# Optimization experiments

Measured on AMD Instinct MI355X. Metric: run time of the kernel, lower is better.

## Reference

```python
import jax, jax.numpy as jnp
import numpy as np

B, N, F_IN = 8, 4096, 32
K = 40          # n_neighbours (includes self, which is dropped)
S = 4           # n_dimensions
P = 22          # n_propagate
F_OUT = 48      # n_filters


def setup_inputs() -> dict:
    key = jax.random.key(0)
    ks = jax.random.split(key, 7)
    def glorot(k, shape):
        fan_in = shape[0]
        return jax.random.normal(k, shape, jnp.float32) / np.sqrt(fan_in)
    x = jax.random.normal(ks[0], (B, N, F_IN), jnp.float32)
    Wf = glorot(ks[1], (F_IN, P)); bf = jnp.zeros((P,), jnp.float32)
    Ws = glorot(ks[2], (F_IN, S)); bs = jnp.zeros((S,), jnp.float32)
    Wo = glorot(ks[3], (F_IN + 2 * P, F_OUT)); bo = jnp.zeros((F_OUT,), jnp.float32)
    return {"x": x, "Wf": Wf, "bf": bf, "Ws": Ws, "bs": bs, "Wo": Wo, "bo": bo}


def reference(x, Wf, bf, Ws, bs, Wo, bo):
    # input transforms
    feats = x @ Wf + bf            # [B, N, P]
    coords = x @ Ws + bs           # [B, N, S]

    # pairwise squared euclidean distances  [B, N, N]
    sq = jnp.sum(coords * coords, axis=-1)
    d2 = sq[:, :, None] + sq[:, None, :] - 2.0 * jnp.einsum('bns,bms->bnm', coords, coords)

    # top-k nearest (top_k of -d2); entry 0 is the vertex itself -> drop it
    neg_d, idx = jax.lax.top_k(-d2, K)          # [B, N, K]
    nidx = idx[:, :, 1:]                         # [B, N, K-1]
    # distance as in TF code: ranked_distances (= -d2 values) sliced
    dist = neg_d[:, :, 1:]                       # negative squared distances

    # gather neighbour features: [B, N, K-1, P]
    neigh = jax.vmap(lambda f, i: f[i])(feats, nidx)

    # gauss_of_lin(dist * 10) = exp(-|dist * 10|)
    w = jnp.exp(-jnp.abs(dist * 10.0))[..., None]
    nf = neigh * w

    agg = jnp.concatenate([jnp.max(nf, axis=2), jnp.mean(nf, axis=2)], axis=-1)  # [B, N, 2P]
    updated = jnp.concatenate([x, agg], axis=-1)                                  # [B, N, F_IN+2P]
    return jnp.tanh(updated @ Wo + bo)                                            # [B, N, F_OUT]
```

## Files before the change

kernel.cpp:

```cpp
#include <hip/hip_runtime.h>
#include <cmath>

#define NN    4096
#define FIN   32
#define KSEL  39
#define PP    22
#define PPAD  24
#define FOUT  48
#define WPB   2
#define QW    4
#define CAP   128
#define WCOLS 32

#define WSYNC() asm volatile("s_waitcnt lgkmcnt(0)" ::: "memory")

__device__ __forceinline__ int lane_prefix(unsigned long long m) {
    return __builtin_amdgcn_mbcnt_hi((unsigned)(m >> 32),
           __builtin_amdgcn_mbcnt_lo((unsigned)m, 0));
}
__device__ __forceinline__ unsigned ford(float f) {
    int u = __float_as_int(f);
    return (u >= 0) ? ((unsigned)u | 0x80000000u) : ~(unsigned)u;
}
__device__ __forceinline__ float funord(unsigned k) {
    unsigned v = (k & 0x80000000u) ? (k & 0x7FFFFFFFu) : ~k;
    return __uint_as_float(v);
}
__device__ __forceinline__ float lane_bcast(float v, int l) {
    return __uint_as_float((unsigned)__builtin_amdgcn_readlane((int)__float_as_uint(v), l));
}
__device__ __forceinline__ float sq4(float4 c) {
    return fmaf(c.x, c.x, fmaf(c.y, c.y, fmaf(c.z, c.z, c.w * c.w)));
}

__global__ __launch_bounds__(256) void gn_pre(
    const float* __restrict__ x,
    const float* __restrict__ Wf, const float* __restrict__ bf,
    const float* __restrict__ Ws, const float* __restrict__ bs,
    float* __restrict__ coords4, float* __restrict__ feats)
{
    __shared__ __align__(16) float sW[FIN * WCOLS];
    __shared__ float sB[WCOLS];

    int t = threadIdx.x;
    for (int idx = t; idx < FIN * WCOLS; idx += 256) {
        int i = idx >> 5, c = idx & 31;
        float v = 0.f;
        if (c < PP) v = Wf[i * PP + c];
        else if (c >= 24 && c < 28) v = Ws[i * 4 + (c - 24)];
        sW[idx] = v;
    }
    if (t < WCOLS) {
        float v = 0.f;
        if (t < PP) v = bf[t];
        else if (t >= 24 && t < 28) v = bs[t - 24];
        sB[t] = v;
    }
    __syncthreads();

    int gid = blockIdx.x * 256 + t;
    int p = gid >> 2;
    int h = gid & 3;
    int c0 = h * 8;

    const float4* xr4 = (const float4*)(x + (size_t)p * FIN);
    float acc[8];
    #pragma unroll
    for (int k = 0; k < 8; ++k) acc[k] = sB[c0 + k];

    #pragma unroll
    for (int i = 0; i < 8; ++i) {
        float4 xt = xr4[i];
        const float* w0 = sW + (4 * i + 0) * WCOLS + c0;
        const float* w1 = sW + (4 * i + 1) * WCOLS + c0;
        const float* w2 = sW + (4 * i + 2) * WCOLS + c0;
        const float* w3 = sW + (4 * i + 3) * WCOLS + c0;
        #pragma unroll
        for (int k = 0; k < 8; ++k) acc[k] = fmaf(xt.x, w0[k], acc[k]);
        #pragma unroll
        for (int k = 0; k < 8; ++k) acc[k] = fmaf(xt.y, w1[k], acc[k]);
        #pragma unroll
        for (int k = 0; k < 8; ++k) acc[k] = fmaf(xt.z, w2[k], acc[k]);
        #pragma unroll
        for (int k = 0; k < 8; ++k) acc[k] = fmaf(xt.w, w3[k], acc[k]);
    }

    if (h < 3) {
        float4* fw = (float4*)(feats + (size_t)p * PPAD + c0);
        fw[0] = make_float4(acc[0], acc[1], acc[2], acc[3]);
        fw[1] = make_float4(acc[4], acc[5], acc[6], acc[7]);
    } else {
        ((float4*)coords4)[p] = make_float4(acc[0], acc[1], acc[2], acc[3]);
    }
}

__device__ __forceinline__ void sort64_pair(float& v, int& m, int lane) {
    #pragma unroll
    for (int k = 2; k <= 64; k <<= 1) {
        #pragma unroll
        for (int j = k >> 1; j >= 1; j >>= 1) {
            float ov = __shfl_xor(v, j);
            int   om = __shfl_xor(m, j);
            bool keepMin = (((lane & j) == 0) == ((lane & k) == 0));
            bool less = (ov < v) || (ov == v && om < m);
            bool take = (less == keepMin);
            v = take ? ov : v;
            m = take ? om : m;
        }
    }
}
__device__ __forceinline__ void merge64(float& Lv, int& Lm, float cv, int cm, int lane) {
    float rv = __shfl_xor(cv, 63);
    int   rm = __shfl_xor(cm, 63);
    bool less = (rv < Lv) || (rv == Lv && rm < Lm);
    if (less) { Lv = rv; Lm = rm; }
    #pragma unroll
    for (int j = 32; j >= 1; j >>= 1) {
        float ov = __shfl_xor(Lv, j);
        int   om = __shfl_xor(Lm, j);
        bool lower = ((lane & j) == 0);
        bool l2 = (ov < Lv) || (ov == Lv && om < Lm);
        bool take = (l2 == lower);
        Lv = take ? ov : Lv;
        Lm = take ? om : Lm;
    }
}

__device__ __forceinline__ float tail_select(
    int lane, int b, int nj, int C,
    const unsigned short* __restrict__ selq,
    const float4* __restrict__ c4,
    const float* __restrict__ feats,
    float* __restrict__ fstage)
{
    const float INF = __builtin_inff();
    float4 cqj = c4[nj];
    float sqnj = sq4(cqj);

    if (C <= CAP) {
        unsigned kd0 = 0xFFFFFFFFu, ki0 = 0xFFFFFFFFu; float dv0 = 0.f;
        if (lane < C) {
            unsigned idx = (unsigned)selq[lane];
            float4 cm = c4[idx];
            float s2 = sq4(cm);
            float dt = fmaf(cqj.x, cm.x, fmaf(cqj.y, cm.y, fmaf(cqj.z, cm.z, cqj.w * cm.w)));
            float d  = fmaxf(fmaf(-2.f, dt, s2 + sqnj), 0.f);
            dv0 = d; kd0 = __float_as_uint(d); ki0 = idx;
        }
        unsigned kd1 = 0xFFFFFFFFu, ki1 = 0xFFFFFFFFu; float dv1 = 0.f;
        if (64 + lane < C) {
            unsigned idx = (unsigned)selq[64 + lane];
            float4 cm = c4[idx];
            float s2 = sq4(cm);
            float dt = fmaf(cqj.x, cm.x, fmaf(cqj.y, cm.y, fmaf(cqj.z, cm.z, cqj.w * cm.w)));
            float d  = fmaxf(fmaf(-2.f, dt, s2 + sqnj), 0.f);
            dv1 = d; kd1 = __float_as_uint(d); ki1 = idx;
        }
        unsigned D = 0;
        for (int bit = 30; bit >= 0; --bit) {
            unsigned t = D | (1u << bit);
            int c = (int)__popcll(__ballot(kd0 < t))
                  + (int)__popcll(__ballot(kd1 < t));
            if (c < KSEL) D = t;
        }
        int cless  = (int)__popcll(__ballot(kd0 < D))
                   + (int)__popcll(__ballot(kd1 < D));
        int tiecnt = (int)__popcll(__ballot(kd0 == D))
                   + (int)__popcll(__ballot(kd1 == D));
        int tneed = KSEL - cless;
        unsigned TI = 0xFFFFFFFFu;
        if (tiecnt > tneed) {
            unsigned pi = 0;
            for (int bit = 11; bit >= 0; --bit) {
                unsigned t = pi | (1u << bit);
                int c = (int)__popcll(__ballot((kd0 == D) && (ki0 < t)))
                      + (int)__popcll(__ballot((kd1 == D) && (ki1 < t)));
                if (c < tneed) pi = t;
            }
            TI = pi;
        }
        bool take0 = (kd0 < D) || ((kd0 == D) && (ki0 <= TI));
        bool take1 = (kd1 < D) || ((kd1 == D) && (ki1 <= TI));
        unsigned long long tb0 = __ballot(take0);
        unsigned long long tb1 = __ballot(take1);
        unsigned base1 = (unsigned)__popcll(tb0);
        if (take0) {
            unsigned slot = (unsigned)lane_prefix(tb0);
            float wgt = __expf(-10.f * dv0);
            const float4* fr = (const float4*)(feats + ((size_t)b * NN + ki0) * PPAD);
            float4 f0 = fr[0], f1 = fr[1], f2 = fr[2], f3 = fr[3], f4 = fr[4], f5 = fr[5];
            float4* row = (float4*)(fstage + slot * PPAD);
            row[0] = make_float4(f0.x * wgt, f0.y * wgt, f0.z * wgt, f0.w * wgt);
            row[1] = make_float4(f1.x * wgt, f1.y * wgt, f1.z * wgt, f1.w * wgt);
            row[2] = make_float4(f2.x * wgt, f2.y * wgt, f2.z * wgt, f2.w * wgt);
            row[3] = make_float4(f3.x * wgt, f3.y * wgt, f3.z * wgt, f3.w * wgt);
            row[4] = make_float4(f4.x * wgt, f4.y * wgt, f4.z * wgt, f4.w * wgt);
            row[5] = make_float4(f5.x * wgt, f5.y * wgt, f5.z * wgt, f5.w * wgt);
        }
        if (take1) {
            unsigned slot = base1 + (unsigned)lane_prefix(tb1);
            float wgt = __expf(-10.f * dv1);
            const float4* fr = (const float4*)(feats + ((size_t)b * NN + ki1) * PPAD);
            float4 f0 = fr[0], f1 = fr[1], f2 = fr[2], f3 = fr[3], f4 = fr[4], f5 = fr[5];
            float4* row = (float4*)(fstage + slot * PPAD);
            row[0] = make_float4(f0.x * wgt, f0.y * wgt, f0.z * wgt, f0.w * wgt);
            row[1] = make_float4(f1.x * wgt, f1.y * wgt, f1.z * wgt, f1.w * wgt);
            row[2] = make_float4(f2.x * wgt, f2.y * wgt, f2.z * wgt, f2.w * wgt);
            row[3] = make_float4(f3.x * wgt, f3.y * wgt, f3.z * wgt, f3.w * wgt);
            row[4] = make_float4(f4.x * wgt, f4.y * wgt, f4.z * wgt, f4.w * wgt);
            row[5] = make_float4(f5.x * wgt, f5.y * wgt, f5.z * wgt, f5.w * wgt);
        }
    } else {
        float Lv = INF; int Lm = 0x7FFFFFFF;
        for (int c = 0; c < 64; ++c) {
            int m = c * 64 + lane;
            float4 cm = c4[m];
            float s2 = sq4(cm);
            float dt = fmaf(cqj.x, cm.x, fmaf(cqj.y, cm.y, fmaf(cqj.z, cm.z, cqj.w * cm.w)));
            float v  = fmaxf(fmaf(-2.f, dt, s2 + sqnj), 0.f);
            if (m == nj) v = INF;
            sort64_pair(v, m, lane);
            if (c == 0) { Lv = v; Lm = m; }
            else        merge64(Lv, Lm, v, m, lane);
        }
        if (lane < KSEL) {
            float wgt = __expf(-10.f * Lv);
            const float4* fr = (const float4*)(feats + ((size_t)b * NN + Lm) * PPAD);
            float4 f0 = fr[0], f1 = fr[1], f2 = fr[2], f3 = fr[3], f4 = fr[4], f5 = fr[5];
            float4* row = (float4*)(fstage + lane * PPAD);
            row[0] = make_float4(f0.x * wgt, f0.y * wgt, f0.z * wgt, f0.w * wgt);
            row[1] = make_float4(f1.x * wgt, f1.y * wgt, f1.z * wgt, f1.w * wgt);
            row[2] = make_float4(f2.x * wgt, f2.y * wgt, f2.z * wgt, f2.w * wgt);
            row[3] = make_float4(f3.x * wgt, f3.y * wgt, f3.z * wgt, f3.w * wgt);
            row[4] = make_float4(f4.x * wgt, f4.y * wgt, f4.z * wgt, f4.w * wgt);
            row[5] = make_float4(f5.x * wgt, f5.y * wgt, f5.z * wgt, f5.w * wgt);
        }
    }
    WSYNC();

    float aggv = 0.f;
    if (lane < 2 * PP) {
        int c = (lane < PP) ? lane : lane - PP;
        float mx = -INF, sm = 0.f;
        for (int k = 0; k < KSEL; ++k) {
            float v = fstage[k * PPAD + c];
            mx = fmaxf(mx, v);
            sm += v;
        }
        aggv = (lane < PP) ? mx : sm * (1.f / (float)KSEL);
    }
    WSYNC();
    return aggv;
}

__global__ __launch_bounds__(WPB * 64, 8) void gn_main(
    const float* __restrict__ x,
    const float* __restrict__ Wo, const float* __restrict__ bo,
    const float* __restrict__ coords4,
    const float* __restrict__ feats,
    float* __restrict__ out)
{
    __shared__ unsigned short sel_s[WPB * QW * CAP];
    __shared__ float fstage_s[WPB * KSEL * PPAD];
    __shared__ unsigned cnt_s[WPB * QW];

    const float INF = __builtin_inff();
    const int wv    = threadIdx.x >> 6;
    const int lane  = threadIdx.x & 63;
    const int qbase = (blockIdx.x * WPB + wv) * QW;
    const int b     = qbase >> 12;
    const int n0    = qbase & (NN - 1);
    unsigned short* selp = sel_s + wv * QW * CAP;
    unsigned* cnt = cnt_s + wv * QW;
    float* fstage = fstage_s + wv * (KSEL * PPAD);

    const float4* c4 = ((const float4*)coords4) + (size_t)b * NN;

    if (lane < QW) cnt[lane] = 0;

    float4 cq0 = c4[n0 + 0], cq1 = c4[n0 + 1], cq2 = c4[n0 + 2], cq3 = c4[n0 + 3];
    float m2x0 = -2.f * cq0.x, m2y0 = -2.f * cq0.y, m2z0 = -2.f * cq0.z, m2w0 = -2.f * cq0.w;
    float m2x1 = -2.f * cq1.x, m2y1 = -2.f * cq1.y, m2z1 = -2.f * cq1.z, m2w1 = -2.f * cq1.w;
    float m2x2 = -2.f * cq2.x, m2y2 = -2.f * cq2.y, m2z2 = -2.f * cq2.z, m2w2 = -2.f * cq2.w;
    float m2x3 = -2.f * cq3.x, m2y3 = -2.f * cq3.y, m2z3 = -2.f * cq3.z, m2w3 = -2.f * cq3.w;

    float km0 = INF, km1 = INF, km2 = INF, km3 = INF;
    #pragma unroll 4
    for (int i = 0; i < 64; ++i) {
        float4 cm = c4[i * 64 + lane];
        float s2  = sq4(cm);
        float e0 = fmaf(m2x0, cm.x, fmaf(m2y0, cm.y, fmaf(m2z0, cm.z, fmaf(m2w0, cm.w, s2))));
        float e1 = fmaf(m2x1, cm.x, fmaf(m2y1, cm.y, fmaf(m2z1, cm.z, fmaf(m2w1, cm.w, s2))));
        float e2 = fmaf(m2x2, cm.x, fmaf(m2y2, cm.y, fmaf(m2z2, cm.z, fmaf(m2w2, cm.w, s2))));
        float e3 = fmaf(m2x3, cm.x, fmaf(m2y3, cm.y, fmaf(m2z3, cm.z, fmaf(m2w3, cm.w, s2))));
        km0 = fminf(km0, e0);
        km1 = fminf(km1, e1);
        km2 = fminf(km2, e2);
        km3 = fminf(km3, e3);
    }
    unsigned kb0 = ford(km0), kb1 = ford(km1), kb2 = ford(km2), kb3 = ford(km3);

    unsigned ub0 = 0, ub1 = 0, ub2 = 0, ub3 = 0;
    for (int bit = 31; bit >= 15; --bit) {
        unsigned msk = 1u << bit;
        unsigned t0 = ub0 | msk, t1 = ub1 | msk, t2 = ub2 | msk, t3 = ub3 | msk;
        if ((int)__popcll(__ballot(kb0 < t0)) < KSEL + 1) ub0 = t0;
        if ((int)__popcll(__ballot(kb1 < t1)) < KSEL + 1) ub1 = t1;
        if ((int)__popcll(__ballot(kb2 < t2)) < KSEL + 1) ub2 = t2;
        if ((int)__popcll(__ballot(kb3 < t3)) < KSEL + 1) ub3 = t3;
    }
    float UBe0 = funord(ub0 | 0x7FFFu);
    float UBe1 = funord(ub1 | 0x7FFFu);
    float UBe2 = funord(ub2 | 0x7FFFu);
    float UBe3 = funord(ub3 | 0x7FFFu);

    const int iSelf = n0 >> 6;
    const int l0    = n0 & 63;
    WSYNC();

    #pragma unroll 4
    for (int i = 0; i < 64; ++i) {
        int m = i * 64 + lane;
        float4 cm = c4[m];
        float s2  = sq4(cm);
        float e0 = fmaf(m2x0, cm.x, fmaf(m2y0, cm.y, fmaf(m2z0, cm.z, fmaf(m2w0, cm.w, s2))));
        float e1 = fmaf(m2x1, cm.x, fmaf(m2y1, cm.y, fmaf(m2z1, cm.z, fmaf(m2w1, cm.w, s2))));
        float e2 = fmaf(m2x2, cm.x, fmaf(m2y2, cm.y, fmaf(m2z2, cm.z, fmaf(m2w2, cm.w, s2))));
        float e3 = fmaf(m2x3, cm.x, fmaf(m2y3, cm.y, fmaf(m2z3, cm.z, fmaf(m2w3, cm.w, s2))));
        bool t0 = (e0 <= UBe0);
        bool t1 = (e1 <= UBe1);
        bool t2 = (e2 <= UBe2);
        bool t3 = (e3 <= UBe3);
        if (i == iSelf) {
            t0 = t0 && (lane != l0 + 0);
            t1 = t1 && (lane != l0 + 1);
            t2 = t2 && (lane != l0 + 2);
            t3 = t3 && (lane != l0 + 3);
        }
        if (t0) {
            unsigned s = atomicAdd(&cnt[0], 1u) & (CAP - 1);
            selp[0 * CAP + s] = (unsigned short)m;
        }
        if (t1) {
            unsigned s = atomicAdd(&cnt[1], 1u) & (CAP - 1);
            selp[1 * CAP + s] = (unsigned short)m;
        }
        if (t2) {
            unsigned s = atomicAdd(&cnt[2], 1u) & (CAP - 1);
            selp[2 * CAP + s] = (unsigned short)m;
        }
        if (t3) {
            unsigned s = atomicAdd(&cnt[3], 1u) & (CAP - 1);
            selp[3 * CAP + s] = (unsigned short)m;
        }
    }
    WSYNC();
    int cc0 = (int)cnt[0];
    int cc1 = (int)cnt[1];
    int cc2 = (int)cnt[2];
    int cc3 = (int)cnt[3];
    WSYNC();

    float agg0 = tail_select(lane, b, n0 + 0, cc0, selp + 0 * CAP, c4, feats, fstage);
    float agg1 = tail_select(lane, b, n0 + 1, cc1, selp + 1 * CAP, c4, feats, fstage);
    float agg2 = tail_select(lane, b, n0 + 2, cc2, selp + 2 * CAP, c4, feats, fstage);
    float agg3 = tail_select(lane, b, n0 + 3, cc3, selp + 3 * CAP, c4, feats, fstage);

    const int qbU = __builtin_amdgcn_readfirstlane(qbase);
    const float* xu = x + (size_t)qbU * FIN;
    if (lane < FOUT) {
        const float* woL = Wo + lane;
        float bb = bo[lane];
        float a00 = bb, a01 = 0.f, a02 = 0.f, a03 = 0.f;
        float a10 = bb, a11 = 0.f, a12 = 0.f, a13 = 0.f;
        float a20 = bb, a21 = 0.f, a22 = 0.f, a23 = 0.f;
        float a30 = bb, a31 = 0.f, a32 = 0.f, a33 = 0.f;
        #pragma unroll
        for (int f = 0; f < FIN; f += 4) {
            float w0 = woL[(f + 0) * FOUT];
            float w1 = woL[(f + 1) * FOUT];
            float w2 = woL[(f + 2) * FOUT];
            float w3 = woL[(f + 3) * FOUT];
            a00 = fmaf(xu[0 * FIN + f + 0], w0, a00);
            a01 = fmaf(xu[0 * FIN + f + 1], w1, a01);
            a02 = fmaf(xu[0 * FIN + f + 2], w2, a02);
            a03 = fmaf(xu[0 * FIN + f + 3], w3, a03);
            a10 = fmaf(xu[1 * FIN + f + 0], w0, a10);
            a11 = fmaf(xu[1 * FIN + f + 1], w1, a11);
            a12 = fmaf(xu[1 * FIN + f + 2], w2, a12);
            a13 = fmaf(xu[1 * FIN + f + 3], w3, a13);
            a20 = fmaf(xu[2 * FIN + f + 0], w0, a20);
            a21 = fmaf(xu[2 * FIN + f + 1], w1, a21);
            a22 = fmaf(xu[2 * FIN + f + 2], w2, a22);
            a23 = fmaf(xu[2 * FIN + f + 3], w3, a23);
            a30 = fmaf(xu[3 * FIN + f + 0], w0, a30);
            a31 = fmaf(xu[3 * FIN + f + 1], w1, a31);
            a32 = fmaf(xu[3 * FIN + f + 2], w2, a32);
            a33 = fmaf(xu[3 * FIN + f + 3], w3, a33);
        }
        #pragma unroll
        for (int g = 0; g < 2 * PP; g += 4) {
            float w0 = woL[(FIN + g + 0) * FOUT];
            float w1 = woL[(FIN + g + 1) * FOUT];
            float w2 = woL[(FIN + g + 2) * FOUT];
            float w3 = woL[(FIN + g + 3) * FOUT];
            a00 = fmaf(lane_bcast(agg0, g + 0), w0, a00);
            a01 = fmaf(lane_bcast(agg0, g + 1), w1, a01);
            a02 = fmaf(lane_bcast(agg0, g + 2), w2, a02);
            a03 = fmaf(lane_bcast(agg0, g + 3), w3, a03);
            a10 = fmaf(lane_bcast(agg1, g + 0), w0, a10);
            a11 = fmaf(lane_bcast(agg1, g + 1), w1, a11);
            a12 = fmaf(lane_bcast(agg1, g + 2), w2, a12);
            a13 = fmaf(lane_bcast(agg1, g + 3), w3, a13);
            a20 = fmaf(lane_bcast(agg2, g + 0), w0, a20);
            a21 = fmaf(lane_bcast(agg2, g + 1), w1, a21);
            a22 = fmaf(lane_bcast(agg2, g + 2), w2, a22);
            a23 = fmaf(lane_bcast(agg2, g + 3), w3, a23);
            a30 = fmaf(lane_bcast(agg3, g + 0), w0, a30);
            a31 = fmaf(lane_bcast(agg3, g + 1), w1, a31);
            a32 = fmaf(lane_bcast(agg3, g + 2), w2, a32);
            a33 = fmaf(lane_bcast(agg3, g + 3), w3, a33);
        }
        float ac0 = (a00 + a01) + (a02 + a03);
        float ac1 = (a10 + a11) + (a12 + a13);
        float ac2 = (a20 + a21) + (a22 + a23);
        float ac3 = (a30 + a31) + (a32 + a33);
        float e0 = __expf(2.f * ac0);
        float e1 = __expf(2.f * ac1);
        float e2 = __expf(2.f * ac2);
        float e3 = __expf(2.f * ac3);
        float r0 = __builtin_amdgcn_rcpf(e0 + 1.f);
        float r1 = __builtin_amdgcn_rcpf(e1 + 1.f);
        float r2 = __builtin_amdgcn_rcpf(e2 + 1.f);
        float r3 = __builtin_amdgcn_rcpf(e3 + 1.f);
        out[(size_t)(qbU + 0) * FOUT + lane] = fmaf(-2.f, r0, 1.f);
        out[(size_t)(qbU + 1) * FOUT + lane] = fmaf(-2.f, r1, 1.f);
        out[(size_t)(qbU + 2) * FOUT + lane] = fmaf(-2.f, r2, 1.f);
        out[(size_t)(qbU + 3) * FOUT + lane] = fmaf(-2.f, r3, 1.f);
    }
}

extern "C" void kernel_launch(void* const* d_in, const int* in_sizes, int n_in,
                              void* d_out, int out_size, void* d_ws, size_t ws_size,
                              hipStream_t stream) {
    const float* x  = (const float*)d_in[0];
    const float* Wf = (const float*)d_in[1];
    const float* bf = (const float*)d_in[2];
    const float* Ws = (const float*)d_in[3];
    const float* bs = (const float*)d_in[4];
    const float* Wo = (const float*)d_in[5];
    const float* bo = (const float*)d_in[6];
    float* outp = (float*)d_out;

    float* ws      = (float*)d_ws;
    float* coords4 = ws;
    float* feats   = ws + 131072;

    gn_pre<<<(32768 * 4) / 256, 256, 0, stream>>>(x, Wf, bf, Ws, bs, coords4, feats);
    gn_main<<<32768 / (WPB * QW), WPB * 64, 0, stream>>>(x, Wo, bo, coords4, feats, outp);
}
```

Before: 148.5 us.

## Interleave tail selection for query pairs with a joint radix-bisection threshold search

Replaces the per-query tail selection with a paired path. Each wave gathers candidate distances for two queries at once, two slots per lane, and runs a shared 31-bit ballot bisection to find each query's 39th-smallest distance threshold. Ties are broken by index, and the selected lists are then compacted into LDS staging for aggregation. Interleaving the two queries is meant to hide ballot and load latency and cut the serial per-query select cost. It adds registers and LDS, and falls back to the old path when a candidate count exceeds the cap.

Result: slower. 169.4 us (+14.1%).

```diff
diff --git a/kernel.cpp b/kernel.cpp
--- a/kernel.cpp
+++ b/kernel.cpp
@@ -253,6 +253,94 @@
     return aggv;
 }
 
+__device__ __forceinline__ void gather_slot(
+    int slotIdx, int C, const unsigned short* __restrict__ selq,
+    const float4* __restrict__ c4, float4 cqj, float sqnj,
+    unsigned& kd, unsigned& ki)
+{
+    kd = 0xFFFFFFFFu; ki = 0xFFFFFFFFu;
+    if (slotIdx < C) {
+        unsigned idx = (unsigned)selq[slotIdx];
+        float4 cm = c4[idx];
+        float s2 = sq4(cm);
+        float dt = fmaf(cqj.x, cm.x, fmaf(cqj.y, cm.y, fmaf(cqj.z, cm.z, cqj.w * cm.w)));
+        float d  = fmaxf(fmaf(-2.f, dt, s2 + sqnj), 0.f);
+        kd = __float_as_uint(d); ki = idx;
+    }
+}
+
+__device__ __forceinline__ void emit_list(
+    unsigned kd0, unsigned ki0, unsigned kd1, unsigned ki1, unsigned D,
+    float2* __restrict__ stg)
+{
+    int cless  = (int)__popcll(__ballot(kd0 < D))
+               + (int)__popcll(__ballot(kd1 < D));
+    int tiecnt = (int)__popcll(__ballot(kd0 == D))
+               + (int)__popcll(__ballot(kd1 == D));
+    int tneed = KSEL - cless;
+    unsigned TI = 0xFFFFFFFFu;
+    if (tiecnt > tneed) {
+        unsigned pi = 0;
+        for (int bit = 11; bit >= 0; --bit) {
+            unsigned t = pi | (1u << bit);
+            int c = (int)__popcll(__ballot((kd0 == D) && (ki0 < t)))
+                  + (int)__popcll(__ballot((kd1 == D) && (ki1 < t)));
+            if (c < tneed) pi = t;
+        }
+        TI = pi;
+    }
+    bool take0 = (kd0 < D) || ((kd0 == D) && (ki0 <= TI));
+    bool take1 = (kd1 < D) || ((kd1 == D) && (ki1 <= TI));
+    unsigned long long tb0 = __ballot(take0);
+    unsigned long long tb1 = __ballot(take1);
+    unsigned base1 = (unsigned)__popcll(tb0);
+    if (take0) {
+        unsigned slot = (unsigned)lane_prefix(tb0);
+        stg[slot] = make_float2(__uint_as_float(kd0), __uint_as_float(ki0));
+    }
+    if (take1) {
+        unsigned slot = base1 + (unsigned)lane_prefix(tb1);
+        stg[slot] = make_float2(__uint_as_float(kd1), __uint_as_float(ki1));
+    }
+}
+
+__device__ __forceinline__ float mat_agg(
+    int lane, int b, const float2* __restrict__ stg,
+    const float* __restrict__ feats, float* __restrict__ fstage)
+{
+    const float INF = __builtin_inff();
+    if (lane < KSEL) {
+        float2 e = stg[lane];
+        float d = e.x;
+        unsigned ki = __float_as_uint(e.y);
+        float wgt = __expf(-10.f * d);
+        const float4* fr = (const float4*)(feats + ((size_t)b * NN + ki) * PPAD);
+        float4 f0 = fr[0], f1 = fr[1], f2 = fr[2], f3 = fr[3], f4 = fr[4], f5 = fr[5];
+        float4* row = (float4*)(fstage + lane * PPAD);
+        row[0] = make_float4(f0.x * wgt, f0.y * wgt, f0.z * wgt, f0.w * wgt);
+        row[1] = make_float4(f1.x * wgt, f1.y * wgt, f1.z * wgt, f1.w * wgt);
+        row[2] = make_float4(f2.x * wgt, f2.y * wgt, f2.z * wgt, f2.w * wgt);
+        row[3] = make_float4(f3.x * wgt, f3.y * wgt, f3.z * wgt, f3.w * wgt);
+        row[4] = make_float4(f4.x * wgt, f4.y * wgt, f4.z * wgt, f4.w * wgt);
+        row[5] = make_float4(f5.x * wgt, f5.y * wgt, f5.z * wgt, f5.w * wgt);
+    }
+    WSYNC();
+
+    float aggv = 0.f;
+    if (lane < 2 * PP) {
+        int c = (lane < PP) ? lane : lane - PP;
+        float mx = -INF, sm = 0.f;
+        for (int k = 0; k < KSEL; ++k) {
+            float v = fstage[k * PPAD + c];
+            mx = fmaxf(mx, v);
+            sm += v;
+        }
+        aggv = (lane < PP) ? mx : sm * (1.f / (float)KSEL);
+    }
+    WSYNC();
+    return aggv;
+}
+
 __global__ __launch_bounds__(WPB * 64, 8) void gn_main(
     const float* __restrict__ x,
     const float* __restrict__ Wo, const float* __restrict__ bo,
@@ -263,6 +351,7 @@
     __shared__ unsigned short sel_s[WPB * QW * CAP];
     __shared__ float fstage_s[WPB * KSEL * PPAD];
     __shared__ unsigned cnt_s[WPB * QW];
+    __shared__ float2 stg_s[WPB * 2 * KSEL];
 
     const float INF = __builtin_inff();
     const int wv    = threadIdx.x >> 6;
@@ -273,6 +362,8 @@
     unsigned short* selp = sel_s + wv * QW * CAP;
     unsigned* cnt = cnt_s + wv * QW;
     float* fstage = fstage_s + wv * (KSEL * PPAD);
+    float2* stgA = stg_s + wv * 2 * KSEL;
+    float2* stgB = stgA + KSEL;
 
     const float4* c4 = ((const float4*)coords4) + (size_t)b * NN;
 
@@ -361,10 +452,59 @@
     int cc3 = (int)cnt[3];
     WSYNC();
 
-    float agg0 = tail_select(lane, b, n0 + 0, cc0, selp + 0 * CAP, c4, feats, fstage);
-    float agg1 = tail_select(lane, b, n0 + 1, cc1, selp + 1 * CAP, c4, feats, fstage);
-    float agg2 = tail_select(lane, b, n0 + 2, cc2, selp + 2 * CAP, c4, feats, fstage);
-    float agg3 = tail_select(lane, b, n0 + 3, cc3, selp + 3 * CAP, c4, feats, fstage);
+    float agg0, agg1, agg2, agg3;
+
+    if (cc0 <= CAP && cc1 <= CAP) {
+        float4 cqa = c4[n0 + 0]; float sqa = sq4(cqa);
+        float4 cqb = c4[n0 + 1]; float sqb = sq4(cqb);
+        unsigned kA0, iA0, kA1, iA1, kB0, iB0, kB1, iB1;
+        gather_slot(lane,      cc0, selp + 0 * CAP, c4, cqa, sqa, kA0, iA0);
+        gather_slot(64 + lane, cc0, selp + 0 * CAP, c4, cqa, sqa, kA1, iA1);
+        gather_slot(lane,      cc1, selp + 1 * CAP, c4, cqb, sqb, kB0, iB0);
+        gather_slot(64 + lane, cc1, selp + 1 * CAP, c4, cqb, sqb, kB1, iB1);
+        unsigned DA = 0, DB = 0;
+        for (int bit = 30; bit >= 0; --bit) {
+            unsigned mA = DA | (1u << bit), mB = DB | (1u << bit);
+            int ca = (int)__popcll(__ballot(kA0 < mA)) + (int)__popcll(__ballot(kA1 < mA));
+            int cb = (int)__popcll(__ballot(kB0 < mB)) + (int)__popcll(__ballot(kB1 < mB));
+            if (ca < KSEL) DA = mA;
+            if (cb < KSEL) DB = mB;
+        }
+        emit_list(kA0, iA0, kA1, iA1, DA, stgA);
+        emit_list(kB0, iB0, kB1, iB1, DB, stgB);
+        WSYNC();
+        agg0 = mat_agg(lane, b, stgA, feats, fstage);
+        agg1 = mat_agg(lane, b, stgB, feats, fstage);
+    } else {
+        agg0 = tail_select(lane, b, n0 + 0, cc0, selp + 0 * CAP, c4, feats, fstage);
+        agg1 = tail_select(lane, b, n0 + 1, cc1, selp + 1 * CAP, c4, feats, fstage);
+    }
+
+    if (cc2 <= CAP && cc3 <= CAP) {
+        float4 cqa = c4[n0 + 2]; float sqa = sq4(cqa);
+        float4 cqb = c4[n0 + 3]; float sqb = sq4(cqb);
+        unsigned kA0, iA0, kA1, iA1, kB0, iB0, kB1, iB1;
+        gather_slot(lane,      cc2, selp + 2 * CAP, c4, cqa, sqa, kA0, iA0);
+        gather_slot(64 + lane, cc2, selp + 2 * CAP, c4, cqa, sqa, kA1, iA1);
+        gather_slot(lane,      cc3, selp + 3 * CAP, c4, cqb, sqb, kB0, iB0);
+        gather_slot(64 + lane, cc3, selp + 3 * CAP, c4, cqb, sqb, kB1, iB1);
+        unsigned DA = 0, DB = 0;
+        for (int bit = 30; bit >= 0; --bit) {
+            unsigned mA = DA | (1u << bit), mB = DB | (1u << bit);
+            int ca = (int)__popcll(__ballot(kA0 < mA)) + (int)__popcll(__ballot(kA1 < mA));
+            int cb = (int)__popcll(__ballot(kB0 < mB)) + (int)__popcll(__ballot(kB1 < mB));
+            if (ca < KSEL) DA = mA;
+            if (cb < KSEL) DB = mB;
+        }
+        emit_list(kA0, iA0, kA1, iA1, DA, stgA);
+        emit_list(kB0, iB0, kB1, iB1, DB, stgB);
+        WSYNC();
+        agg2 = mat_agg(lane, b, stgA, feats, fstage);
+        agg3 = mat_agg(lane, b, stgB, feats, fstage);
+    } else {
+        agg2 = tail_select(lane, b, n0 + 2, cc2, selp + 2 * CAP, c4, feats, fstage);
+        agg3 = tail_select(lane, b, n0 + 3, cc3, selp + 3 * CAP, c4, feats, fstage);
+    }
 
     const int qbU = __builtin_amdgcn_readfirstlane(qbase);
     const float* xu = x + (size_t)qbU * FIN;
```
